# Kernel tuning notes

Hardware: AMD Instinct MI355X
Metric: run time of the kernel (lower is better)

## Reference

```python
import jax, jax.numpy as jnp
import numpy as np

NEG_FILL = -100.0  # matches torch new_full(-100.0) init for scatter-amax


def reference(x, part_labels, parts_num=16):
    # x: (n, c, s, h, w) float; part_labels: (n, s, h, w) int in [0, parts_num)
    n, c, s, h, w = x.shape
    hw = h * w
    ns = n * s
    # (n s) c (h w)
    feat = jnp.transpose(x, (0, 2, 1, 3, 4)).reshape(ns, c, hw)
    labels = part_labels.reshape(ns, hw).astype(jnp.int32)

    b3 = jnp.arange(ns)[:, None, None]          # (ns,1,1)
    ch = jnp.arange(c)[None, :, None]            # (1,c,1)
    lbl3 = labels[:, None, :]                    # (ns,1,hw) -> broadcasts to (ns,c,hw)

    pooled_sum = jnp.zeros((ns, c, parts_num), x.dtype).at[b3, ch, lbl3].add(feat)
    b2 = jnp.arange(ns)[:, None]
    pooled_count = jnp.zeros((ns, parts_num), x.dtype).at[b2, labels].add(1.0)  # (ns,P)
    pooled_max = jnp.full((ns, c, parts_num), NEG_FILL, x.dtype).at[b3, ch, lbl3].max(feat)

    count = pooled_count[:, None, :]             # (ns,1,P)
    pooled_mean = pooled_sum / jnp.maximum(count, 1.0)
    pooled_max = jnp.where(count > 0, pooled_max, 0.0)
    pooled = pooled_mean + pooled_max            # (ns,c,P)
    # (n s) c p -> n c s p
    return jnp.transpose(pooled.reshape(n, s, c, parts_num), (0, 2, 1, 3))


def setup_inputs() -> dict:
    key = jax.random.key(0)
    k1, k2 = jax.random.split(key)
    n, c, s, h, w = 16, 256, 32, 16, 11
    parts_num = 16
    x = jax.random.normal(k1, (n, c, s, h, w), dtype=jnp.float32)
    part_labels = jax.random.randint(k2, (n, s, h, w), 0, parts_num, dtype=jnp.int64)
    return {"x": x, "part_labels": part_labels, "parts_num": parts_num}
```

## Files before the change

kernel.cpp:

```cpp
#include <hip/hip_runtime.h>


constexpr int C   = 256;
constexpr int S   = 32;
constexpr int HW  = 176;
constexpr int P   = 16;
constexpr int ROW = S * HW;
constexpr int GC  = 8;
constexpr int NS2 = 2;
constexpr int PITCH = 178;
constexpr int BCAP  = 64;
constexpr int PPITCH = 68;
constexpr float NEG_FILL = -100.0f;

__device__ __forceinline__ void barrier_lgkm() {
    asm volatile("s_waitcnt lgkmcnt(0)\n\ts_barrier" ::: "memory");
}

__global__ __launch_bounds__(256) void hpp_kernel(
    const float* __restrict__ x,
    const int*   __restrict__ labels,
    float*       __restrict__ out)
{
    __shared__ float         tile[GC * NS2 * PITCH];
    __shared__ unsigned char perm[NS2 * P * PPITCH];
    __shared__ int           cnt[NS2 * P];

    const int tid = threadIdx.x;
    const int blk = blockIdx.x;
    const int nsp = blk >> 5, cg = blk & 31;
    const int n   = nsp >> 4, sp = nsp & 15;
    const int s   = sp * 2;

    const int* ln = labels + (size_t)(n * S + s) * HW;
    int lab0 = 0, lab1 = 0;
    if (tid < HW) { lab0 = ln[tid]; lab1 = ln[HW + tid]; }

    const float* xb = x + (size_t)(n * C + cg * GC) * ROW + s * HW;
    const int f0 = tid, f1 = tid + 256, f2 = tid + 512;
    const int r0 = f0 / 88, j0 = f0 - r0 * 88;
    const int r1 = f1 / 88, j1 = f1 - r1 * 88;
    const int r2 = f2 / 88, j2 = f2 - r2 * 88;
    float4 v0 = *(const float4*)(xb + (size_t)r0 * ROW + j0 * 4);
    float4 v1 = *(const float4*)(xb + (size_t)r1 * ROW + j1 * 4);
    float4 v2 = make_float4(0.f, 0.f, 0.f, 0.f);
    const bool has2 = (f2 < GC * 88);
    if (has2) v2 = *(const float4*)(xb + (size_t)r2 * ROW + j2 * 4);

    if (tid < NS2 * P) cnt[tid] = 0;
    barrier_lgkm();
    if (tid < HW) {
        int a = atomicAdd(&cnt[lab0], 1);
        if (a < BCAP) perm[lab0 * PPITCH + a] = (unsigned char)tid;
        int b = atomicAdd(&cnt[P + lab1], 1);
        if (b < BCAP) perm[P * PPITCH + lab1 * PPITCH + b] = (unsigned char)tid;
    }
    barrier_lgkm();

    {
        const int q0 = j0 * 4, s20 = (q0 >= HW), h0 = q0 - s20 * HW;
        float2* t0 = (float2*)&tile[(r0 * 2 + s20) * PITCH + h0];
        t0[0] = make_float2(v0.x, v0.y); t0[1] = make_float2(v0.z, v0.w);

        const int q1 = j1 * 4, s21 = (q1 >= HW), h1 = q1 - s21 * HW;
        float2* t1 = (float2*)&tile[(r1 * 2 + s21) * PITCH + h1];
        t1[0] = make_float2(v1.x, v1.y); t1[1] = make_float2(v1.z, v1.w);

        if (has2) {
            const int q2 = j2 * 4, s22 = (q2 >= HW), h2 = q2 - s22 * HW;
            float2* t2 = (float2*)&tile[(r2 * 2 + s22) * PITCH + h2];
            t2[0] = make_float2(v2.x, v2.y); t2[1] = make_float2(v2.z, v2.w);
        }
    }
    barrier_lgkm();

    const int p   = tid >> 4;
    const int low = tid & 15;
    const int sp2 = low & 1;
    const int c   = low >> 1;
    const int k   = min(cnt[sp2 * P + p], BCAP);
    const unsigned char* pp = &perm[(sp2 * P + p) * PPITCH];
    const float*         tc = &tile[low * PITCH];

    float s0 = 0.f, s1 = 0.f, m0 = NEG_FILL, m1 = NEG_FILL;
    const int kf = k & ~3;
    for (int j = 0; j < kf; j += 4) {
        unsigned u = *(const unsigned*)&pp[j];
        float a0 = tc[u & 0xFF];
        float a1 = tc[(u >> 8) & 0xFF];
        float a2 = tc[(u >> 16) & 0xFF];
        float a3 = tc[u >> 24];
        s0 += a0; m0 = fmaxf(m0, a0);
        s1 += a1; m1 = fmaxf(m1, a1);
        s0 += a2; m0 = fmaxf(m0, a2);
        s1 += a3; m1 = fmaxf(m1, a3);
    }
    if (kf < k) {
        unsigned u = *(const unsigned*)&pp[kf];
        float a0 = tc[u & 0xFF];
        float a1 = tc[(u >> 8) & 0xFF];
        float a2 = tc[(u >> 16) & 0xFF];
        s0 += a0; m0 = fmaxf(m0, a0);
        if (kf + 1 < k) { s1 += a1; m1 = fmaxf(m1, a1); }
        if (kf + 2 < k) { s0 += a2; m0 = fmaxf(m0, a2); }
    }

    float res = (k > 0) ? (s0 + s1) / (float)k + fmaxf(m0, m1) : 0.f;
    out[((size_t)(n * C + cg * GC + c) * S + (s + sp2)) * P + p] = res;
}

extern "C" void kernel_launch(void* const* d_in, const int* in_sizes, int n_in,
                              void* d_out, int out_size, void* d_ws, size_t ws_size,
                              hipStream_t stream) {
    const float* x      = (const float*)d_in[0];
    const int*   labels = (const int*)d_in[1];
    float*       out    = (float*)d_out;

    const int ns_total = in_sizes[1] / HW;
    const int nblk     = (ns_total / NS2) * (C / GC);
    hpp_kernel<<<nblk, 256, 0, stream>>>(x, labels, out);
}
```

Measured before the change: 136.1 us.

## Scatter tile into label-sorted order via prefix-sum positions, reduce contiguous runs

Replaces the per-part index list (perm) with a counting sort: counts per label, a prefix sum gives each part's base offset, and each pixel's destination position is stored in a byte map. Input values are scattered into the shared tile in label-grouped order, so the reduction phase reads contiguous runs with float4 loads instead of gathering through byte indices. It also drops the BCAP cap on parts, so overflowing parts are now handled correctly. The cost is two extra barriers, a serial prefix loop in 32 threads, and scattered scalar LDS stores in place of float2 stores.

```diff
diff --git a/kernel.cpp b/kernel.cpp
--- a/kernel.cpp
+++ b/kernel.cpp
@@ -8,9 +8,7 @@
 constexpr int ROW = S * HW;
 constexpr int GC  = 8;
 constexpr int NS2 = 2;
-constexpr int PITCH = 178;
-constexpr int BCAP  = 64;
-constexpr int PPITCH = 68;
+constexpr int PITCH = 180;
 constexpr float NEG_FILL = -100.0f;
 
 __device__ __forceinline__ void barrier_lgkm() {
@@ -22,9 +20,10 @@
     const int*   __restrict__ labels,
     float*       __restrict__ out)
 {
-    __shared__ float         tile[GC * NS2 * PITCH];
-    __shared__ unsigned char perm[NS2 * P * PPITCH];
-    __shared__ int           cnt[NS2 * P];
+    __shared__ float tile[GC * NS2 * PITCH];
+    __shared__ __align__(4) unsigned char posmap[NS2][HW];
+    __shared__ int cnt[NS2 * P];
+    __shared__ int base[NS2 * P];
 
     const int tid = threadIdx.x;
     const int blk = blockIdx.x;
@@ -49,27 +48,44 @@
 
     if (tid < NS2 * P) cnt[tid] = 0;
     barrier_lgkm();
+    int a0 = 0, a1 = 0;
     if (tid < HW) {
-        int a = atomicAdd(&cnt[lab0], 1);
-        if (a < BCAP) perm[lab0 * PPITCH + a] = (unsigned char)tid;
-        int b = atomicAdd(&cnt[P + lab1], 1);
-        if (b < BCAP) perm[P * PPITCH + lab1 * PPITCH + b] = (unsigned char)tid;
+        a0 = atomicAdd(&cnt[lab0], 1);
+        a1 = atomicAdd(&cnt[P + lab1], 1);
+    }
+    barrier_lgkm();
+    if (tid < NS2 * P) {
+        int acc = 0;
+        const int b0 = tid & ~(P - 1);
+        for (int q = b0; q < tid; ++q) acc += cnt[q];
+        base[tid] = acc;
+    }
+    barrier_lgkm();
+    if (tid < HW) {
+        posmap[0][tid] = (unsigned char)(base[lab0] + a0);
+        posmap[1][tid] = (unsigned char)(base[P + lab1] + a1);
     }
     barrier_lgkm();
 
     {
         const int q0 = j0 * 4, s20 = (q0 >= HW), h0 = q0 - s20 * HW;
-        float2* t0 = (float2*)&tile[(r0 * 2 + s20) * PITCH + h0];
-        t0[0] = make_float2(v0.x, v0.y); t0[1] = make_float2(v0.z, v0.w);
+        unsigned pm0 = *(const unsigned*)&posmap[s20][h0];
+        float* t0 = &tile[(r0 * 2 + s20) * PITCH];
+        t0[pm0 & 0xFF] = v0.x; t0[(pm0 >> 8) & 0xFF] = v0.y;
+        t0[(pm0 >> 16) & 0xFF] = v0.z; t0[pm0 >> 24] = v0.w;
 
         const int q1 = j1 * 4, s21 = (q1 >= HW), h1 = q1 - s21 * HW;
-        float2* t1 = (float2*)&tile[(r1 * 2 + s21) * PITCH + h1];
-        t1[0] = make_float2(v1.x, v1.y); t1[1] = make_float2(v1.z, v1.w);
+        unsigned pm1 = *(const unsigned*)&posmap[s21][h1];
+        float* t1 = &tile[(r1 * 2 + s21) * PITCH];
+        t1[pm1 & 0xFF] = v1.x; t1[(pm1 >> 8) & 0xFF] = v1.y;
+        t1[(pm1 >> 16) & 0xFF] = v1.z; t1[pm1 >> 24] = v1.w;
 
         if (has2) {
             const int q2 = j2 * 4, s22 = (q2 >= HW), h2 = q2 - s22 * HW;
-            float2* t2 = (float2*)&tile[(r2 * 2 + s22) * PITCH + h2];
-            t2[0] = make_float2(v2.x, v2.y); t2[1] = make_float2(v2.z, v2.w);
+            unsigned pm2 = *(const unsigned*)&posmap[s22][h2];
+            float* t2 = &tile[(r2 * 2 + s22) * PITCH];
+            t2[pm2 & 0xFF] = v2.x; t2[(pm2 >> 8) & 0xFF] = v2.y;
+            t2[(pm2 >> 16) & 0xFF] = v2.z; t2[pm2 >> 24] = v2.w;
         }
     }
     barrier_lgkm();
@@ -78,32 +94,31 @@
     const int low = tid & 15;
     const int sp2 = low & 1;
     const int c   = low >> 1;
-    const int k   = min(cnt[sp2 * P + p], BCAP);
-    const unsigned char* pp = &perm[(sp2 * P + p) * PPITCH];
-    const float*         tc = &tile[low * PITCH];
+    const int idx = sp2 * P + p;
+    const int k   = cnt[idx];
+    int off       = base[idx];
+    const float* tc = &tile[low * PITCH];
 
     float s0 = 0.f, s1 = 0.f, m0 = NEG_FILL, m1 = NEG_FILL;
-    const int kf = k & ~3;
-    for (int j = 0; j < kf; j += 4) {
-        unsigned u = *(const unsigned*)&pp[j];
-        float a0 = tc[u & 0xFF];
-        float a1 = tc[(u >> 8) & 0xFF];
-        float a2 = tc[(u >> 16) & 0xFF];
-        float a3 = tc[u >> 24];
-        s0 += a0; m0 = fmaxf(m0, a0);
-        s1 += a1; m1 = fmaxf(m1, a1);
-        s0 += a2; m0 = fmaxf(m0, a2);
-        s1 += a3; m1 = fmaxf(m1, a3);
+    int rem = k;
+    int h = (4 - (off & 3)) & 3; if (h > rem) h = rem;
+    if (h > 0) { float a = tc[off];     s0 += a; m0 = fmaxf(m0, a); }
+    if (h > 1) { float a = tc[off + 1]; s1 += a; m1 = fmaxf(m1, a); }
+    if (h > 2) { float a = tc[off + 2]; s0 += a; m0 = fmaxf(m0, a); }
+    off += h; rem -= h;
+    int n4 = rem >> 2;
+    for (int i = 0; i < n4; ++i) {
+        float4 q = *(const float4*)&tc[off];
+        s0 += q.x; m0 = fmaxf(m0, q.x);
+        s1 += q.y; m1 = fmaxf(m1, q.y);
+        s0 += q.z; m0 = fmaxf(m0, q.z);
+        s1 += q.w; m1 = fmaxf(m1, q.w);
+        off += 4;
     }
-    if (kf < k) {
-        unsigned u = *(const unsigned*)&pp[kf];
-        float a0 = tc[u & 0xFF];
-        float a1 = tc[(u >> 8) & 0xFF];
-        float a2 = tc[(u >> 16) & 0xFF];
-        s0 += a0; m0 = fmaxf(m0, a0);
-        if (kf + 1 < k) { s1 += a1; m1 = fmaxf(m1, a1); }
-        if (kf + 2 < k) { s0 += a2; m0 = fmaxf(m0, a2); }
-    }
+    rem &= 3;
+    if (rem > 0) { float a = tc[off];     s0 += a; m0 = fmaxf(m0, a); }
+    if (rem > 1) { float a = tc[off + 1]; s1 += a; m1 = fmaxf(m1, a); }
+    if (rem > 2) { float a = tc[off + 2]; s0 += a; m0 = fmaxf(m0, a); }
 
     float res = (k > 0) ? (s0 + s1) / (float)k + fmaxf(m0, m1) : 0.f;
     out[((size_t)(n * C + cg * GC + c) * S + (s + sp2)) * P + p] = res;
```

Result: no change. 136.3 us (+0.2%).
